# Kernel tuning notes

Measured on AMD Instinct MI355X. Metric: run time of the kernel, lower is better.

## Reference

```python
import jax, jax.numpy as jnp
import numpy as np

ALPHA = 2.0  # spikingjelly surrogate.Erf default alpha

@jax.custom_vjp
def erf_spike(x):
    # spiking forward: heaviside(x); backward uses Erf surrogate gradient
    return (x >= 0).astype(x.dtype)

def _erf_spike_fwd(x):
    return erf_spike(x), x

def _erf_spike_bwd(x, g):
    return (g * jnp.exp(-(x * ALPHA) ** 2) * (ALPHA / np.sqrt(np.pi)),)

erf_spike.defvjp(_erf_spike_fwd, _erf_spike_bwd)

L, T, B, C, H, N_LAYERS = 256, 4, 32, 256, 256, 2

def setup_inputs() -> dict:
    key = jax.random.key(0)
    ks = jax.random.split(key, 8)
    k = 1.0 / np.sqrt(H)  # uniform(-sqrt(1/H), sqrt(1/H)) init
    u = lambda kk, shape: jax.random.uniform(kk, shape, jnp.float32, -k, k)
    return {
        "x": jax.random.normal(ks[0], (L, T, B, C), jnp.float32),
        "W_ih0": u(ks[1], (4 * H, C)),
        "W_hh0": u(ks[2], (4 * H, H)),
        "b0": u(ks[3], (4 * H,)),
        "W_ih1": u(ks[4], (4 * H, H)),
        "W_hh1": u(ks[5], (4 * H, H)),
        "b1": u(ks[6], (4 * H,)),
    }

def _run_layer(inp, W_ih, W_hh, b):
    # inp: [L, T, B, Cin] -> fold T,B into one batch axis for the scan
    Ls, Ts, Bs = inp.shape[0], inp.shape[1], inp.shape[2]
    Hs = W_hh.shape[1]
    xin = inp.reshape(Ls, Ts * Bs, -1)

    def step(carry, x_t):
        h, c = carry
        gates = x_t @ W_ih.T + h @ W_hh.T + b  # [TB, 4H]
        i, f, g, o = jnp.split(gates, 4, axis=-1)
        i = erf_spike(i)
        f = erf_spike(f)
        g = erf_spike(g)
        o = erf_spike(o)
        c = f * c + i * g
        # torch.clamp_max_ under no_grad: value clamp, straight-through grad
        c = c + jax.lax.stop_gradient(jnp.minimum(c, 1.0) - c)
        h = o * c
        return (h, c), h

    h0 = jnp.zeros((Ts * Bs, Hs), inp.dtype)
    (h, c), out = jax.lax.scan(step, (h0, h0), xin)
    return (out.reshape(Ls, Ts, Bs, Hs),
            h.reshape(Ts, Bs, Hs),
            c.reshape(Ts, Bs, Hs))

def reference(x, W_ih0, W_hh0, b0, W_ih1, W_hh1, b1):
    out0, h0, c0 = _run_layer(x, W_ih0, W_hh0, b0)
    out1, h1, c1 = _run_layer(out0, W_ih1, W_hh1, b1)
    state_h = jnp.stack([h0, h1])  # [N, T, B, H]
    state_c = jnp.stack([c0, c1])
    return out1, (state_h, state_c)
```

## Files before the change

### kernel.cpp

```cpp
#include <hip/hip_runtime.h>
#include <math.h>

typedef _Float16 half8 __attribute__((ext_vector_type(8)));
typedef _Float16 half4v __attribute__((ext_vector_type(4)));
typedef float floatx4 __attribute__((ext_vector_type(4)));
typedef unsigned long long u64;

#define MFMA16(a, b, c) __builtin_amdgcn_mfma_f32_16x16x32_f16((a), (b), (c), 0, 0, 0)
#define AARG __ATOMIC_RELAXED, __HIP_MEMORY_SCOPE_AGENT

static constexpr float C11 = 4.8828125e-4f;
static constexpr int SLOTS = 257;
static constexpr int LSTRIDE = SLOTS * 8 * 128;

__device__ u64 g_exch[2 * LSTRIDE];
__device__ _Float16 g_xhi[8388608];
__device__ _Float16 g_xlo[8388608];
__device__ float g_phi[33554432];
__device__ _Float16 g_plo[33554432];
__device__ unsigned g_done;

__global__ __launch_bounds__(256) void zero_k() {
  unsigned i = blockIdx.x * 256 + threadIdx.x;
  if (i < 2 * LSTRIDE) g_exch[i] = 0;
  if (i == 0) g_done = 0;
}

__device__ __forceinline__ u64 ald(const u64* p) { return __hip_atomic_load(p, AARG); }
__device__ __forceinline__ void ast(u64* p, u64 v) { __hip_atomic_store(p, v, AARG); }

__device__ __forceinline__ void barrier_lds() {
  __builtin_amdgcn_sched_barrier(0);
  asm volatile("s_waitcnt lgkmcnt(0)" ::: "memory");
  __builtin_amdgcn_s_barrier();
  __builtin_amdgcn_sched_barrier(0);
}

__device__ __forceinline__ void split16(float v, _Float16& hi, _Float16& lo) {
  _Float16 h = (fabsf(v) < 6.103515625e-05f) ? (_Float16)0.0f : (_Float16)v;
  hi = h;
  lo = (_Float16)((v - (float)h) * 2048.0f);
}

__global__ __launch_bounds__(256) void presplit_k(const float* __restrict__ x) {
  int i = (blockIdx.x * 256 + threadIdx.x) * 8;
  floatx4 a = *(const floatx4*)(x + i);
  floatx4 b = *(const floatx4*)(x + i + 4);
  half8 hi, lo;
#pragma unroll
  for (int e = 0; e < 4; ++e) { _Float16 p, q; split16(a[e], p, q); hi[e] = p; lo[e] = q; }
#pragma unroll
  for (int e = 0; e < 4; ++e) { _Float16 p, q; split16(b[e], p, q); hi[4 + e] = p; lo[4 + e] = q; }
  *(half8*)(g_xhi + i) = hi;
  *(half8*)(g_xlo + i) = lo;
}

__global__ __launch_bounds__(256) void gemm0_k(const float* __restrict__ wih) {
  const int tid = threadIdx.x, lane = tid & 63, wv = tid >> 6;
  const int m16 = lane & 15, l16 = lane >> 4;
  const int bi = blockIdx.x;
  const int lc = bi >> 6, g = (bi >> 3) & 7, kwg = bi & 7;

  half8 WH[2][8], WL[2][8];
#pragma unroll
  for (int t2 = 0; t2 < 2; ++t2) {
    int grow = wv * 256 + 32 * kwg + t2 * 16 + m16;
#pragma unroll
    for (int q = 0; q < 8; ++q) {
      const float* src = wih + (size_t)grow * 256 + 32 * q + 8 * l16;
      floatx4 v0 = *(const floatx4*)src;
      floatx4 v1 = *(const floatx4*)(src + 4);
      half8 hi, lo;
#pragma unroll
      for (int e = 0; e < 4; ++e) { _Float16 p, q2; split16(v0[e], p, q2); hi[e] = p; lo[e] = q2; }
#pragma unroll
      for (int e = 0; e < 4; ++e) { _Float16 p, q2; split16(v1[e], p, q2); hi[4 + e] = p; lo[4 + e] = q2; }
      WH[t2][q] = hi;
      WL[t2][q] = lo;
    }
  }
#pragma unroll 1
  for (int l = lc * 32; l < lc * 32 + 32; ++l) {
    size_t base = ((size_t)l * 128 + 16 * g + m16) * 256 + 8 * l16;
    half8 xh[8], xl[8];
#pragma unroll
    for (int q = 0; q < 8; ++q) {
      xh[q] = *(const half8*)(g_xhi + base + 32 * q);
      xl[q] = *(const half8*)(g_xlo + base + 32 * q);
    }
    floatx4 zz = {0.f, 0.f, 0.f, 0.f};
    floatx4 A0[2], A1[2], A2[2];
    A0[0] = A0[1] = zz; A1[0] = A1[1] = zz; A2[0] = A2[1] = zz;
#pragma unroll
    for (int q = 0; q < 8; ++q)
#pragma unroll
      for (int t2 = 0; t2 < 2; ++t2) {
        A0[t2] = MFMA16(xh[q], WH[t2][q], A0[t2]);
        A1[t2] = MFMA16(xh[q], WL[t2][q], A1[t2]);
        A1[t2] = MFMA16(xl[q], WH[t2][q], A1[t2]);
        A2[t2] = MFMA16(xl[q], WL[t2][q], A2[t2]);
      }
#pragma unroll
    for (int t2 = 0; t2 < 2; ++t2) {
      size_t off = ((((((size_t)l * 8 + g) * 8 + kwg) * 4 + wv) * 2 + t2) * 64 + lane) * 4;
      *(floatx4*)(g_phi + off) = A0[t2];
      half4v hv;
#pragma unroll
      for (int r = 0; r < 4; ++r) hv[r] = (_Float16)(A1[t2][r] + C11 * A2[t2][r]);
      *(half4v*)(g_plo + off) = hv;
    }
  }
}

template <int LAYER>
__device__ void scan_body(_Float16* lut, float* ihb, unsigned* hw, u64* spike,
                          const float* __restrict__ wih,
                          const float* __restrict__ whh,
                          const float* __restrict__ bias,
                          float* __restrict__ dout, int g, int kwg) {
  const int tid = threadIdx.x;
  const int lane = tid & 63;
  const int wv = tid >> 6;
  const bool prod = wv < 4;
  const int gate = wv & 3;
  const int m16 = lane & 15;
  const int l16 = lane >> 4;

  u64* exch0 = g_exch;
  u64* exchMy = g_exch + LAYER * LSTRIDE;

  if (tid < 256) {
#pragma unroll
    for (int e = 0; e < 8; ++e)
      lut[tid * 8 + e] = ((tid >> e) & 1) ? (_Float16)1.0f : (_Float16)0.0f;
  }

  half8 FH[2][8], FL[2][8];
  if (!prod || LAYER == 1) {
    const float* wsrc = prod ? wih : whh;
#pragma unroll
    for (int t2 = 0; t2 < 2; ++t2) {
      int grow = gate * 256 + 32 * kwg + t2 * 16 + m16;
#pragma unroll
      for (int q = 0; q < 8; ++q) {
        const float* src = wsrc + (size_t)grow * 256 + 32 * q + 8 * l16;
        floatx4 v0 = *(const floatx4*)src;
        floatx4 v1 = *(const floatx4*)(src + 4);
        half8 hi, lo;
#pragma unroll
        for (int e = 0; e < 4; ++e) { _Float16 p, q2; split16(v0[e], p, q2); hi[e] = p; lo[e] = q2; }
#pragma unroll
        for (int e = 0; e < 4; ++e) { _Float16 p, q2; split16(v1[e], p, q2); hi[4 + e] = p; lo[4 + e] = q2; }
        FH[t2][q] = hi;
        FL[t2][q] = lo;
      }
    }
  }
  float bl[2];
#pragma unroll
  for (int t2 = 0; t2 < 2; ++t2) bl[t2] = bias[gate * 256 + 32 * kwg + t2 * 16 + m16];

  floatx4 ihA0[2], ihA1[2];
  floatx4 phv[2];
  half4v plv[2];
  u64 xwA[8];
  unsigned xw[8];
  u64 cst = 0;
  int polls = 0;
  const int POLL_MAX = 1 << 22;

  auto issue_pl = [&](int l) {
#pragma unroll
    for (int t2 = 0; t2 < 2; ++t2) {
      size_t off = ((((((size_t)l * 8 + g) * 8 + kwg) * 4 + gate) * 2 + t2) * 64 + lane) * 4;
      phv[t2] = *(const floatx4*)(g_phi + off);
      plv[t2] = *(const half4v*)(g_plo + off);
    }
  };
  auto issue_xw = [&](int tag) {
    const u64* page = exch0 + (size_t)tag * 1024 + g * 128 + m16;
#pragma unroll
    for (int q = 0; q < 8; ++q) xwA[q] = ald(page + q * 16);
  };
  auto consume_xw = [&](int tag) {
    bool ok = true;
#pragma unroll
    for (int q = 0; q < 8; ++q) ok = ok && ((unsigned)xwA[q] == (unsigned)tag);
    if (!__all(ok)) {
      const u64* page = exch0 + (size_t)tag * 1024 + g * 128 + m16;
      for (;;) {
#pragma unroll
        for (int q = 0; q < 8; ++q) xwA[q] = ald(page + q * 16);
        bool k2 = true;
#pragma unroll
        for (int q = 0; q < 8; ++q) k2 = k2 && ((unsigned)xwA[q] == (unsigned)tag);
        if (__all(k2)) break;
        if (++polls > POLL_MAX) break;
      }
    }
#pragma unroll
    for (int q = 0; q < 8; ++q) xw[q] = (unsigned)(xwA[q] >> 32);
  };
  auto ih_mfma = [&]() {
    floatx4 zz = {0.f, 0.f, 0.f, 0.f};
    ihA0[0] = ihA0[1] = zz;
    ihA1[0] = ihA1[1] = zz;
#pragma unroll
    for (int q = 0; q < 8; ++q) {
      unsigned byt = (xw[q] >> (8 * l16)) & 0xFFu;
      half8 ah = *(const half8*)(lut + byt * 8);
#pragma unroll
      for (int t2 = 0; t2 < 2; ++t2) {
        ihA0[t2] = MFMA16(ah, FH[t2][q], ihA0[t2]);
        ihA1[t2] = MFMA16(ah, FL[t2][q], ihA1[t2]);
      }
    }
  };
  auto gather16 = [&](u64 v) -> unsigned {
    unsigned a0 = __shfl((unsigned)v, lane & 3);
    unsigned a1 = __shfl((unsigned)(v >> 32), lane & 3);
    unsigned b0 = __shfl((unsigned)v, 4 + (lane & 3));
    unsigned b1 = __shfl((unsigned)(v >> 32), 4 + (lane & 3));
    u64 A = ((u64)a1 << 32) | a0;
    u64 B = ((u64)b1 << 32) | b0;
    int sh = 16 * ((lane & 15) >> 2);
    return (unsigned)((A >> sh) & 0xFFFFull) |
           ((unsigned)((B >> sh) & 0xFFFFull) << 16);
  };

  if (prod) {
    if constexpr (LAYER == 0) {
      issue_pl(0);
    } else {
      issue_xw(1);
      consume_xw(1);
      ih_mfma();
      issue_xw(2);
    }
  }
  __syncthreads();

#pragma unroll 1
  for (int l = 0; l < 256; ++l) {
    if (prod) {
#pragma unroll
      for (int t2 = 0; t2 < 2; ++t2) {
        float* b2 = ihb + ((gate * 2 + t2) * 8) * 64 + lane;
        if constexpr (LAYER == 0) {
#pragma unroll
          for (int r = 0; r < 4; ++r) {
            b2[r * 64] = phv[t2][r];
            b2[(4 + r) * 64] = (float)plv[t2][r];
          }
        } else {
#pragma unroll
          for (int r = 0; r < 4; ++r) {
            b2[r * 64] = ihA0[t2][r];
            b2[(4 + r) * 64] = ihA1[t2][r];
          }
        }
      }
    } else if (wv == 4 && l > 0) {
      const u64* pa = exchMy + (size_t)l * 1024 + g * 128 + 2 * lane;
      u64 v0 = ald(pa), v1 = ald(pa + 1);
      for (;;) {
        if (__all(((unsigned)v0 == (unsigned)l) && ((unsigned)v1 == (unsigned)l))) break;
        v0 = ald(pa);
        v1 = ald(pa + 1);
        if (++polls > POLL_MAX) break;
      }
      hw[2 * lane] = (unsigned)(v0 >> 32);
      hw[2 * lane + 1] = (unsigned)(v1 >> 32);
    }
    barrier_lds();
    if (prod) {
      if (l < 255) {
        if constexpr (LAYER == 0) {
          issue_pl(l + 1);
        } else {
          consume_xw(l + 2);
          ih_mfma();
          if (l + 3 <= 256) issue_xw(l + 3);
        }
      }
    } else {
      floatx4 C0[2], C1[2];
#pragma unroll
      for (int t2 = 0; t2 < 2; ++t2) {
        const float* b2 = ihb + ((gate * 2 + t2) * 8) * 64 + lane;
#pragma unroll
        for (int r = 0; r < 4; ++r) {
          C0[t2][r] = b2[r * 64];
          C1[t2][r] = b2[(4 + r) * 64];
        }
      }
      if (l > 0) {
#pragma unroll
        for (int q = 0; q < 8; ++q) {
          unsigned mw = hw[q * 16 + m16];
          unsigned byt = (mw >> (8 * l16)) & 0xFFu;
          half8 af = *(const half8*)(lut + byt * 8);
          C0[0] = MFMA16(af, FH[0][q], C0[0]);
          C0[1] = MFMA16(af, FH[1][q], C0[1]);
          C1[0] = MFMA16(af, FL[0][q], C1[0]);
          C1[1] = MFMA16(af, FL[1][q], C1[1]);
        }
      }
      u64 bal[2][4];
#pragma unroll
      for (int r = 0; r < 4; ++r) {
        float p0 = C0[0][r] + bl[0] + C11 * C1[0][r];
        float p1 = C0[1][r] + bl[1] + C11 * C1[1][r];
        bal[0][r] = __ballot(p0 >= 0.0f);
        bal[1][r] = __ballot(p1 >= 0.0f);
      }
      if (lane == 0) {
#pragma unroll
        for (int t2 = 0; t2 < 2; ++t2)
#pragma unroll
          for (int r = 0; r < 4; ++r) spike[gate * 8 + t2 * 4 + r] = bal[t2][r];
      }
    }
    barrier_lds();
    {
      int idx = lane & 7;
      u64 iS = spike[idx], fS = spike[8 + idx];
      u64 gS = spike[16 + idx];
      cst = (fS & cst) | (iS & gS);
    }
    u64 hS = spike[24 + (lane & 7)] & cst;
    if (wv == 0) {
      unsigned hu = gather16(hS);
      if (lane < 16)
        ast(exchMy + (size_t)(l + 1) * 1024 + g * 128 + kwg * 16 + lane,
            ((u64)hu << 32) | (unsigned)(l + 1));
    }
    if (LAYER == 1 && wv == 1) {
      unsigned hu = gather16(hS);
      if (lane < 16) {
        float* frow = dout + ((size_t)l * 128 + 16 * g + lane) * 256 + 32 * kwg;
#pragma unroll
        for (int c4 = 0; c4 < 8; ++c4) {
          floatx4 v;
#pragma unroll
          for (int j = 0; j < 4; ++j) v[j] = ((hu >> (c4 * 4 + j)) & 1) ? 1.0f : 0.0f;
          *(floatx4*)(frow + c4 * 4) = v;
        }
      }
    }
    if (l == 255 && wv == 2) {
      unsigned hu = gather16(hS);
      unsigned cu = gather16(cst);
      if (lane < 16) {
        float* shp = dout + 8388608 + LAYER * 32768 +
                     (size_t)(16 * g + lane) * 256 + 32 * kwg;
        float* scp = shp + 65536;
#pragma unroll
        for (int c4 = 0; c4 < 8; ++c4) {
          floatx4 vh, vc;
#pragma unroll
          for (int j = 0; j < 4; ++j) {
            vh[j] = ((hu >> (c4 * 4 + j)) & 1) ? 1.0f : 0.0f;
            vc[j] = ((cu >> (c4 * 4 + j)) & 1) ? 1.0f : 0.0f;
          }
          *(floatx4*)(shp + c4 * 4) = vh;
          *(floatx4*)(scp + c4 * 4) = vc;
        }
      }
    }
  }
  __syncthreads();
  if (tid == 0)
    __hip_atomic_fetch_add(&g_done, 1u, __ATOMIC_RELAXED, __HIP_MEMORY_SCOPE_AGENT);
}

__global__ __launch_bounds__(512, 2) void spike_scan(
    const float* __restrict__ wih1, const float* __restrict__ whh0,
    const float* __restrict__ whh1, const float* __restrict__ b0,
    const float* __restrict__ b1, float* __restrict__ dout) {
  __shared__ __align__(16) _Float16 lut[256 * 8];
  __shared__ __align__(16) float ihb[4 * 2 * 8 * 64];
  __shared__ unsigned hw[128];
  __shared__ u64 spike[32];

  int bi = blockIdx.x;
  if (bi >= 128) {
    float a0 = (float)threadIdx.x * 0.001f + 1.0f;
    float a1 = a0 + 0.1f, a2 = a0 + 0.2f, a3 = a0 + 0.3f;
    float a4 = a0 + 0.4f, a5 = a0 + 0.5f, a6 = a0 + 0.6f, a7 = a0 + 0.7f;
    half8 hb;
#pragma unroll
    for (int e = 0; e < 8; ++e) hb[e] = (_Float16)0.5f;
    floatx4 acc = {0.f, 0.f, 0.f, 0.f};
#pragma unroll 1
    for (int it = 0; it < 8192; ++it) {
#pragma unroll
      for (int k = 0; k < 64; ++k) {
        a0 = __builtin_fmaf(a0, 1.0000001f, 1e-7f);
        a1 = __builtin_fmaf(a1, 1.0000001f, 1e-7f);
        a2 = __builtin_fmaf(a2, 1.0000001f, 1e-7f);
        a3 = __builtin_fmaf(a3, 1.0000001f, 1e-7f);
        a4 = __builtin_fmaf(a4, 1.0000001f, 1e-7f);
        a5 = __builtin_fmaf(a5, 1.0000001f, 1e-7f);
        a6 = __builtin_fmaf(a6, 1.0000001f, 1e-7f);
        a7 = __builtin_fmaf(a7, 1.0000001f, 1e-7f);
      }
      acc = MFMA16(hb, hb, acc);
      if (__hip_atomic_load(&g_done, __ATOMIC_RELAXED, __HIP_MEMORY_SCOPE_AGENT) >= 128u)
        break;
    }
    asm volatile("" ::"v"(a0), "v"(a1), "v"(a2), "v"(a3), "v"(a4), "v"(a5),
                 "v"(a6), "v"(a7), "v"(acc[0]));
    return;
  }
  int g = bi & 7;
  int kwg = (bi >> 3) & 7;
  if ((bi >> 6) == 0)
    scan_body<0>(lut, ihb, hw, spike, (const float*)nullptr, whh0, b0, dout, g, kwg);
  else
    scan_body<1>(lut, ihb, hw, spike, wih1, whh1, b1, dout, g, kwg);
}

extern "C" void kernel_launch(void* const* d_in, const int* in_sizes, int n_in,
                              void* d_out, int out_size, void* d_ws, size_t ws_size,
                              hipStream_t stream) {
  (void)in_sizes; (void)n_in; (void)out_size; (void)d_ws; (void)ws_size;
  const float* x = (const float*)d_in[0];
  const float* wih0 = (const float*)d_in[1];
  const float* whh0 = (const float*)d_in[2];
  const float* b0 = (const float*)d_in[3];
  const float* wih1 = (const float*)d_in[4];
  const float* whh1 = (const float*)d_in[5];
  const float* b1 = (const float*)d_in[6];
  float* dout = (float*)d_out;

  zero_k<<<2056, 256, 0, stream>>>();
  presplit_k<<<4096, 256, 0, stream>>>(x);
  gemm0_k<<<512, 256, 0, stream>>>(wih0);
  spike_scan<<<256, 512, 0, stream>>>(wih1, whh0, whh1, b0, b1, dout);
}
```

Measured before the change: 634.3 us.

## Fuse layer-0 input projection GEMM into scan producer waves

Removes the separate gemm0_k pre-pass and its large fp32/fp16 intermediate buffers. Layer-0 producer waves now load the split x tiles and compute the input-projection MFMAs inline, one step ahead, with register-held W_ih0 splits. This avoids writing and reading about 200MB of precomputed gate partials, but puts the extra MFMA work on the scan's per-step critical path and raises register pressure in the producer waves.

```diff
diff --git a/kernel.cpp b/kernel.cpp
--- a/kernel.cpp
+++ b/kernel.cpp
@@ -2,7 +2,6 @@
 #include <math.h>
 
 typedef _Float16 half8 __attribute__((ext_vector_type(8)));
-typedef _Float16 half4v __attribute__((ext_vector_type(4)));
 typedef float floatx4 __attribute__((ext_vector_type(4)));
 typedef unsigned long long u64;
 
@@ -16,8 +15,6 @@
 __device__ u64 g_exch[2 * LSTRIDE];
 __device__ _Float16 g_xhi[8388608];
 __device__ _Float16 g_xlo[8388608];
-__device__ float g_phi[33554432];
-__device__ _Float16 g_plo[33554432];
 __device__ unsigned g_done;
 
 __global__ __launch_bounds__(256) void zero_k() {
@@ -53,63 +50,6 @@
   for (int e = 0; e < 4; ++e) { _Float16 p, q; split16(b[e], p, q); hi[4 + e] = p; lo[4 + e] = q; }
   *(half8*)(g_xhi + i) = hi;
   *(half8*)(g_xlo + i) = lo;
-}
-
-__global__ __launch_bounds__(256) void gemm0_k(const float* __restrict__ wih) {
-  const int tid = threadIdx.x, lane = tid & 63, wv = tid >> 6;
-  const int m16 = lane & 15, l16 = lane >> 4;
-  const int bi = blockIdx.x;
-  const int lc = bi >> 6, g = (bi >> 3) & 7, kwg = bi & 7;
-
-  half8 WH[2][8], WL[2][8];
-#pragma unroll
-  for (int t2 = 0; t2 < 2; ++t2) {
-    int grow = wv * 256 + 32 * kwg + t2 * 16 + m16;
-#pragma unroll
-    for (int q = 0; q < 8; ++q) {
-      const float* src = wih + (size_t)grow * 256 + 32 * q + 8 * l16;
-      floatx4 v0 = *(const floatx4*)src;
-      floatx4 v1 = *(const floatx4*)(src + 4);
-      half8 hi, lo;
-#pragma unroll
-      for (int e = 0; e < 4; ++e) { _Float16 p, q2; split16(v0[e], p, q2); hi[e] = p; lo[e] = q2; }
-#pragma unroll
-      for (int e = 0; e < 4; ++e) { _Float16 p, q2; split16(v1[e], p, q2); hi[4 + e] = p; lo[4 + e] = q2; }
-      WH[t2][q] = hi;
-      WL[t2][q] = lo;
-    }
-  }
-#pragma unroll 1
-  for (int l = lc * 32; l < lc * 32 + 32; ++l) {
-    size_t base = ((size_t)l * 128 + 16 * g + m16) * 256 + 8 * l16;
-    half8 xh[8], xl[8];
-#pragma unroll
-    for (int q = 0; q < 8; ++q) {
-      xh[q] = *(const half8*)(g_xhi + base + 32 * q);
-      xl[q] = *(const half8*)(g_xlo + base + 32 * q);
-    }
-    floatx4 zz = {0.f, 0.f, 0.f, 0.f};
-    floatx4 A0[2], A1[2], A2[2];
-    A0[0] = A0[1] = zz; A1[0] = A1[1] = zz; A2[0] = A2[1] = zz;
-#pragma unroll
-    for (int q = 0; q < 8; ++q)
-#pragma unroll
-      for (int t2 = 0; t2 < 2; ++t2) {
-        A0[t2] = MFMA16(xh[q], WH[t2][q], A0[t2]);
-        A1[t2] = MFMA16(xh[q], WL[t2][q], A1[t2]);
-        A1[t2] = MFMA16(xl[q], WH[t2][q], A1[t2]);
-        A2[t2] = MFMA16(xl[q], WL[t2][q], A2[t2]);
-      }
-#pragma unroll
-    for (int t2 = 0; t2 < 2; ++t2) {
-      size_t off = ((((((size_t)l * 8 + g) * 8 + kwg) * 4 + wv) * 2 + t2) * 64 + lane) * 4;
-      *(floatx4*)(g_phi + off) = A0[t2];
-      half4v hv;
-#pragma unroll
-      for (int r = 0; r < 4; ++r) hv[r] = (_Float16)(A1[t2][r] + C11 * A2[t2][r]);
-      *(half4v*)(g_plo + off) = hv;
-    }
-  }
 }
 
 template <int LAYER>
@@ -136,7 +76,7 @@
   }
 
   half8 FH[2][8], FL[2][8];
-  if (!prod || LAYER == 1) {
+  {
     const float* wsrc = prod ? wih : whh;
 #pragma unroll
     for (int t2 = 0; t2 < 2; ++t2) {
@@ -161,21 +101,41 @@
   for (int t2 = 0; t2 < 2; ++t2) bl[t2] = bias[gate * 256 + 32 * kwg + t2 * 16 + m16];
 
   floatx4 ihA0[2], ihA1[2];
-  floatx4 phv[2];
-  half4v plv[2];
+  half8 xrh[8], xrl[8];
   u64 xwA[8];
   unsigned xw[8];
   u64 cst = 0;
   int polls = 0;
   const int POLL_MAX = 1 << 22;
 
-  auto issue_pl = [&](int l) {
-#pragma unroll
-    for (int t2 = 0; t2 < 2; ++t2) {
-      size_t off = ((((((size_t)l * 8 + g) * 8 + kwg) * 4 + gate) * 2 + t2) * 64 + lane) * 4;
-      phv[t2] = *(const floatx4*)(g_phi + off);
-      plv[t2] = *(const half4v*)(g_plo + off);
-    }
+  auto issue_x = [&](int ln) {
+    size_t base = ((size_t)ln * 128 + 16 * g + m16) * 256 + 8 * l16;
+#pragma unroll
+    for (int q = 0; q < 8; ++q) {
+      xrh[q] = *(const half8*)(g_xhi + base + 32 * q);
+      xrl[q] = *(const half8*)(g_xlo + base + 32 * q);
+    }
+  };
+  auto ihx_mfma = [&]() {
+    floatx4 zz = {0.f, 0.f, 0.f, 0.f};
+    floatx4 A2[2];
+    ihA0[0] = ihA0[1] = zz;
+    ihA1[0] = ihA1[1] = zz;
+    A2[0] = A2[1] = zz;
+#pragma unroll
+    for (int q = 0; q < 8; ++q)
+#pragma unroll
+      for (int t2 = 0; t2 < 2; ++t2) {
+        ihA0[t2] = MFMA16(xrh[q], FH[t2][q], ihA0[t2]);
+        ihA1[t2] = MFMA16(xrh[q], FL[t2][q], ihA1[t2]);
+        ihA1[t2] = MFMA16(xrl[q], FH[t2][q], ihA1[t2]);
+        A2[t2] = MFMA16(xrl[q], FL[t2][q], A2[t2]);
+      }
+#pragma unroll
+    for (int t2 = 0; t2 < 2; ++t2)
+#pragma unroll
+      for (int r = 0; r < 4; ++r)
+        ihA1[t2][r] = (float)(_Float16)(ihA1[t2][r] + C11 * A2[t2][r]);
   };
   auto issue_xw = [&](int tag) {
     const u64* page = exch0 + (size_t)tag * 1024 + g * 128 + m16;
@@ -230,7 +190,9 @@
 
   if (prod) {
     if constexpr (LAYER == 0) {
-      issue_pl(0);
+      issue_x(0);
+      ihx_mfma();
+      issue_x(1);
     } else {
       issue_xw(1);
       consume_xw(1);
@@ -246,18 +208,10 @@
 #pragma unroll
       for (int t2 = 0; t2 < 2; ++t2) {
         float* b2 = ihb + ((gate * 2 + t2) * 8) * 64 + lane;
-        if constexpr (LAYER == 0) {
-#pragma unroll
-          for (int r = 0; r < 4; ++r) {
-            b2[r * 64] = phv[t2][r];
-            b2[(4 + r) * 64] = (float)plv[t2][r];
-          }
-        } else {
-#pragma unroll
-          for (int r = 0; r < 4; ++r) {
-            b2[r * 64] = ihA0[t2][r];
-            b2[(4 + r) * 64] = ihA1[t2][r];
-          }
+#pragma unroll
+        for (int r = 0; r < 4; ++r) {
+          b2[r * 64] = ihA0[t2][r];
+          b2[(4 + r) * 64] = ihA1[t2][r];
         }
       }
     } else if (wv == 4 && l > 0) {
@@ -276,7 +230,8 @@
     if (prod) {
       if (l < 255) {
         if constexpr (LAYER == 0) {
-          issue_pl(l + 1);
+          ihx_mfma();
+          issue_x(l + 2 > 255 ? 255 : l + 2);
         } else {
           consume_xw(l + 2);
           ih_mfma();
@@ -375,9 +330,10 @@
 }
 
 __global__ __launch_bounds__(512, 2) void spike_scan(
-    const float* __restrict__ wih1, const float* __restrict__ whh0,
-    const float* __restrict__ whh1, const float* __restrict__ b0,
-    const float* __restrict__ b1, float* __restrict__ dout) {
+    const float* __restrict__ wih0, const float* __restrict__ wih1,
+    const float* __restrict__ whh0, const float* __restrict__ whh1,
+    const float* __restrict__ b0, const float* __restrict__ b1,
+    float* __restrict__ dout) {
   __shared__ __align__(16) _Float16 lut[256 * 8];
   __shared__ __align__(16) float ihb[4 * 2 * 8 * 64];
   __shared__ unsigned hw[128];
@@ -416,7 +372,7 @@
   int g = bi & 7;
   int kwg = (bi >> 3) & 7;
   if ((bi >> 6) == 0)
-    scan_body<0>(lut, ihb, hw, spike, (const float*)nullptr, whh0, b0, dout, g, kwg);
+    scan_body<0>(lut, ihb, hw, spike, wih0, whh0, b0, dout, g, kwg);
   else
     scan_body<1>(lut, ihb, hw, spike, wih1, whh1, b1, dout, g, kwg);
 }
@@ -436,6 +392,5 @@
 
   zero_k<<<2056, 256, 0, stream>>>();
   presplit_k<<<4096, 256, 0, stream>>>(x);
-  gemm0_k<<<512, 256, 0, stream>>>(wih0);
-  spike_scan<<<256, 512, 0, stream>>>(wih1, whh0, whh1, b0, b1, dout);
-}
+  spike_scan<<<256, 512, 0, stream>>>(wih0, wih1, whh0, whh1, b0, b1, dout);
+}
```

New measurement: 876.8 us. 1.38x slower.
